# Performance work log

Measured on AMD Instinct MI355X. Metric: run time of the kernel, lower is better.

## Reference

```python
import jax, jax.numpy as jnp
import numpy as np

N_ATOMS = 100000
N_EDGES = 6400000
R_MAX = 6.0


def setup_inputs() -> dict:
    key = jax.random.key(0)
    k1, k2, k3 = jax.random.split(key, 3)
    R = jax.random.normal(k1, (N_ATOMS, 3), dtype=jnp.float32) * 10.0
    Z = jax.random.randint(k2, (N_ATOMS,), 1, 50, dtype=jnp.int32)
    idx = jax.random.randint(k3, (2, N_EDGES), 0, N_ATOMS, dtype=jnp.int32)
    # learned params (values per nn.initializers.constant in setup())
    a_exp = jnp.full((1,), 0.23, dtype=jnp.float32)
    a_num = jnp.full((1,), 0.4685, dtype=jnp.float32)
    coefficients = jnp.array([0.18175, 0.50986, 0.28022, 0.02817], dtype=jnp.float32)[:, None]
    exponents = jnp.array([3.1998, 0.94229, 0.4029, 0.20162], dtype=jnp.float32)[:, None]
    return {"R": R, "Z": Z, "idx": idx, "a_exp": a_exp, "a_num": a_num,
            "coefficients": coefficients, "exponents": exponents}


def reference(R, Z, idx, a_exp, a_num, coefficients, exponents):
    n_atoms = R.shape[0]
    idx_i, idx_j = idx[0], idx[1]
    Zf = Z.astype(R.dtype)
    Z_i, Z_j = Zf[idx_i], Zf[idx_j]                       # [E]
    dr_vec = R[idx_j] - R[idx_i]                          # free-space displacement [E,3]
    dr = jnp.sqrt(jnp.sum(dr_vec * dr_vec, axis=-1))      # [E]
    dr = jnp.clip(dr, 0.02, R_MAX)
    cos_cutoff = 0.5 * (jnp.cos(jnp.pi * dr / R_MAX) + 1.0)
    a_divisor = Z_i ** a_exp[0] + Z_j ** a_exp[0]
    dist = dr * a_divisor / a_num[0]                      # [E]
    f = jnp.sum(coefficients * jnp.exp(-exponents * dist), axis=0)  # (4,1)x[E]->(4,E)->[E]
    E_ij = 0.5 * Z_i * Z_j / dr * f * cos_cutoff          # [E]
    # mask_by_neighbor: padded edges carry idx == n_atoms -> zero contribution
    valid = (idx_i < n_atoms) & (idx_j < n_atoms)
    E_ij = jnp.where(valid, E_ij, 0.0)
    return jnp.sum(E_ij)
```

## Files before the change

### kernel.cpp

```cpp
#include <hip/hip_runtime.h>
#include <math.h>

#define N_ATOMS 100000
#define N_EDGES 6400000
#define NZB 50000
#define TBL_BYTES (N_ATOMS * 16)
#define XY_OFF    TBL_BYTES
#define Z_OFF     (XY_OFF + N_ATOMS)
#define WS_NEED   (Z_OFF + NZB)

__device__ __forceinline__ int cell6(float x) {
    return min(max((int)((x + 48.0f) * (1.0f / 6.0f)), 0), 15);
}

__global__ __launch_bounds__(256)
void build_tables(const float* __restrict__ R, const int* __restrict__ Z,
                  float4* __restrict__ P, unsigned char* __restrict__ gxy,
                  unsigned char* __restrict__ gz) {
    int i = blockIdx.x * blockDim.x + threadIdx.x;
    if (i < N_ATOMS) {
        float x = R[3 * i], y = R[3 * i + 1], z = R[3 * i + 2];
        P[i] = make_float4(x, y, z, (float)Z[i]);
        gxy[i] = (unsigned char)(cell6(x) | (cell6(y) << 4));
    }
    if (i < NZB) {
        int a0 = 2 * i, a1 = 2 * i + 1;
        int c0 = cell6(R[3 * a0 + 2]);
        int c1 = (a1 < N_ATOMS) ? cell6(R[3 * a1 + 2]) : 0;
        gz[i] = (unsigned char)(c0 | (c1 << 4));
    }
}

__global__ __launch_bounds__(1024)
void zbl_prefilter(const float4* __restrict__ P,
                   const unsigned char* __restrict__ gxy,
                   const unsigned char* __restrict__ gz,
                   const int*    __restrict__ idx,
                   const float*  __restrict__ a_exp,
                   const float*  __restrict__ a_num,
                   const float*  __restrict__ coef,
                   const float*  __restrict__ expo,
                   float*        __restrict__ out)
{
    __shared__ __align__(16) unsigned char sxy[N_ATOMS];
    __shared__ __align__(16) unsigned char sz[NZB];
    __shared__ float powz[64];
    __shared__ float wave_part[16];

    const int t = threadIdx.x;

    {
        const uint4* s = (const uint4*)gxy;
        uint4*       d = (uint4*)sxy;
        for (int k = t; k < N_ATOMS / 16; k += 1024) d[k] = s[k];
        const uint4* s2 = (const uint4*)gz;
        uint4*       d2 = (uint4*)sz;
        for (int k = t; k < NZB / 16; k += 1024) d2[k] = s2[k];
    }

    const float aexp     = a_exp[0];
    const float inv_anum = 1.0f / a_num[0];
    const float c0 = coef[0], c1 = coef[1], c2 = coef[2], c3 = coef[3];
    const float e0 = expo[0], e1 = expo[1], e2 = expo[2], e3 = expo[3];
    if (t < 64) powz[t] = __powf((float)t, aexp);
    __syncthreads();

    const int4* idx_i4 = (const int4*)idx;
    const int4* idx_j4 = (const int4*)(idx + N_EDGES);
    const int n4 = N_EDGES / 4;
    const int tid    = blockIdx.x * blockDim.x + t;
    const int stride = gridDim.x * blockDim.x;

    const float PI_OVER_RMAX = 0.52359877559829887f;

    float acc = 0.0f;
    for (int k = tid; k < n4; k += stride) {
        int4 ii = idx_i4[k];
        int4 jj = idx_j4[k];

        unsigned ia[4], jb[4];
        bool pass[4];
#pragma unroll
        for (int u = 0; u < 4; ++u) {
            int i = (&ii.x)[u];
            int j = (&jj.x)[u];
            bool valid = ((unsigned)i < N_ATOMS) & ((unsigned)j < N_ATOMS);
            unsigned a = min((unsigned)i, N_ATOMS - 1u);
            unsigned b = min((unsigned)j, N_ATOMS - 1u);
            ia[u] = a; jb[u] = b;
            int ci = sxy[a], cj = sxy[b];
            int dxy = abs((ci & 15) - (cj & 15)) | abs((ci >> 4) - (cj >> 4));
            pass[u] = valid & (dxy <= 1);
        }
#pragma unroll
        for (int u = 0; u < 4; ++u) {
            if (pass[u]) {
                unsigned a = ia[u], b = jb[u];
                int zi = (sz[a >> 1] >> ((a & 1) << 2)) & 15;
                int zj = (sz[b >> 1] >> ((b & 1) << 2)) & 15;
                if (abs(zi - zj) <= 1) {
                    float4 pa = P[a];
                    float4 pb = P[b];
                    float dx = pb.x - pa.x, dy = pb.y - pa.y, dz = pb.z - pa.z;
                    float d2 = dx * dx + dy * dy + dz * dz;
                    if (d2 < 36.0f) {
                        float dr = fmaxf(sqrtf(d2), 0.02f);
                        int za = (int)pa.w, zb = (int)pb.w;
                        float dist = dr * (powz[za & 63] + powz[zb & 63]) * inv_anum;
                        float f = c0 * __expf(-e0 * dist) + c1 * __expf(-e1 * dist)
                                + c2 * __expf(-e2 * dist) + c3 * __expf(-e3 * dist);
                        float cc = 0.5f * (__cosf(PI_OVER_RMAX * dr) + 1.0f);
                        acc += 0.5f * pa.w * pb.w / dr * f * cc;
                    }
                }
            }
        }
    }

#pragma unroll
    for (int off = 32; off > 0; off >>= 1)
        acc += __shfl_down(acc, off, 64);
    const int lane = t & 63;
    const int wave = t >> 6;
    if (lane == 0) wave_part[wave] = acc;
    __syncthreads();
    if (t == 0) {
        float s = 0.0f;
#pragma unroll
        for (int w = 0; w < 16; ++w) s += wave_part[w];
        atomicAdd(out, s);
    }
}

__global__ __launch_bounds__(256)
void zbl_mlp(const float4* __restrict__ P, const int* __restrict__ idx,
             const float* __restrict__ a_exp, const float* __restrict__ a_num,
             const float* __restrict__ coef, const float* __restrict__ expo,
             float* __restrict__ out)
{
    __shared__ float powz[64];
    __shared__ float wave_part[4];
    const float aexp = a_exp[0];
    const float inv_anum = 1.0f / a_num[0];
    const float c0 = coef[0], c1 = coef[1], c2 = coef[2], c3 = coef[3];
    const float e0 = expo[0], e1 = expo[1], e2 = expo[2], e3 = expo[3];
    const int t = threadIdx.x;
    if (t < 64) powz[t] = __powf((float)t, aexp);
    __syncthreads();
    const int4* idx_i4 = (const int4*)idx;
    const int4* idx_j4 = (const int4*)(idx + N_EDGES);
    const int n4 = N_EDGES / 4;
    const int tid = blockIdx.x * blockDim.x + t;
    const int stride = gridDim.x * blockDim.x;
    const float PI_OVER_RMAX = 0.52359877559829887f;
    float acc = 0.0f;
    for (int k = tid; k < n4; k += stride) {
        int4 ii = idx_i4[k];
        int4 jj = idx_j4[k];
        float4 pa[4], pb[4];
        bool valid[4];
#pragma unroll
        for (int u = 0; u < 4; ++u) {
            int i = (&ii.x)[u], j = (&jj.x)[u];
            valid[u] = ((unsigned)i < N_ATOMS) & ((unsigned)j < N_ATOMS);
            pa[u] = P[min((unsigned)i, N_ATOMS - 1u)];
            pb[u] = P[min((unsigned)j, N_ATOMS - 1u)];
        }
#pragma unroll
        for (int u = 0; u < 4; ++u) {
            float dx = pb[u].x - pa[u].x, dy = pb[u].y - pa[u].y, dz = pb[u].z - pa[u].z;
            float d2 = dx * dx + dy * dy + dz * dz;
            if (valid[u] && d2 < 36.0f) {
                float dr = fmaxf(sqrtf(d2), 0.02f);
                int zi = (int)pa[u].w, zj = (int)pb[u].w;
                float dist = dr * (powz[zi & 63] + powz[zj & 63]) * inv_anum;
                float f = c0 * __expf(-e0 * dist) + c1 * __expf(-e1 * dist)
                        + c2 * __expf(-e2 * dist) + c3 * __expf(-e3 * dist);
                float cc = 0.5f * (__cosf(PI_OVER_RMAX * dr) + 1.0f);
                acc += 0.5f * pa[u].w * pb[u].w / dr * f * cc;
            }
        }
    }
#pragma unroll
    for (int off = 32; off > 0; off >>= 1)
        acc += __shfl_down(acc, off, 64);
    const int lane = t & 63, wave = t >> 6;
    if (lane == 0) wave_part[wave] = acc;
    __syncthreads();
    if (t == 0)
        atomicAdd(out, wave_part[0] + wave_part[1] + wave_part[2] + wave_part[3]);
}

extern "C" void kernel_launch(void* const* d_in, const int* in_sizes, int n_in,
                              void* d_out, int out_size, void* d_ws, size_t ws_size,
                              hipStream_t stream) {
    const float* R     = (const float*)d_in[0];
    const int*   Z     = (const int*)d_in[1];
    const int*   idx   = (const int*)d_in[2];
    const float* a_exp = (const float*)d_in[3];
    const float* a_num = (const float*)d_in[4];
    const float* coef  = (const float*)d_in[5];
    const float* expo  = (const float*)d_in[6];
    float* out = (float*)d_out;

    hipMemsetAsync(out, 0, sizeof(float), stream);

    if (ws_size >= (size_t)WS_NEED) {
        float4*        P   = (float4*)d_ws;
        unsigned char* gxy = (unsigned char*)d_ws + XY_OFF;
        unsigned char* gz  = (unsigned char*)d_ws + Z_OFF;
        build_tables<<<(N_ATOMS + 255) / 256, 256, 0, stream>>>(R, Z, P, gxy, gz);
        zbl_prefilter<<<256, 1024, 0, stream>>>(P, gxy, gz, idx,
                                                a_exp, a_num, coef, expo, out);
    } else if (ws_size >= (size_t)TBL_BYTES) {
        float4* P = (float4*)d_ws;
        build_tables<<<(N_ATOMS + 255) / 256, 256, 0, stream>>>(
            R, Z, P, (unsigned char*)d_ws, (unsigned char*)d_ws);
        zbl_mlp<<<2048, 256, 0, stream>>>(P, idx, a_exp, a_num, coef, expo, out);
    }
}
```

Baseline: 122.0 us.

## Compact surviving edges into per-wave LDS queue to remove divergence

Drops the z-cell prefilter table and replaces the divergent per-lane evaluation with a per-wave ring queue in shared memory. Edges that pass the xy-cell test are compacted using ballot and popcount, and once 64 entries are queued the whole wave evaluates them together. This is meant to avoid running the costly exp/cos path with most lanes idle. In exchange it adds ballot and LDS traffic for every edge group, uses more shared memory, and sends more candidates to the full distance test because the z filter is gone.

```diff
diff --git a/kernel.cpp b/kernel.cpp
--- a/kernel.cpp
+++ b/kernel.cpp
@@ -3,11 +3,9 @@
 
 #define N_ATOMS 100000
 #define N_EDGES 6400000
-#define NZB 50000
 #define TBL_BYTES (N_ATOMS * 16)
 #define XY_OFF    TBL_BYTES
-#define Z_OFF     (XY_OFF + N_ATOMS)
-#define WS_NEED   (Z_OFF + NZB)
+#define WS_NEED   (XY_OFF + N_ATOMS)
 
 __device__ __forceinline__ int cell6(float x) {
     return min(max((int)((x + 48.0f) * (1.0f / 6.0f)), 0), 15);
@@ -15,35 +13,27 @@
 
 __global__ __launch_bounds__(256)
 void build_tables(const float* __restrict__ R, const int* __restrict__ Z,
-                  float4* __restrict__ P, unsigned char* __restrict__ gxy,
-                  unsigned char* __restrict__ gz) {
+                  float4* __restrict__ P, unsigned char* __restrict__ gxy) {
     int i = blockIdx.x * blockDim.x + threadIdx.x;
     if (i < N_ATOMS) {
         float x = R[3 * i], y = R[3 * i + 1], z = R[3 * i + 2];
         P[i] = make_float4(x, y, z, (float)Z[i]);
         gxy[i] = (unsigned char)(cell6(x) | (cell6(y) << 4));
     }
-    if (i < NZB) {
-        int a0 = 2 * i, a1 = 2 * i + 1;
-        int c0 = cell6(R[3 * a0 + 2]);
-        int c1 = (a1 < N_ATOMS) ? cell6(R[3 * a1 + 2]) : 0;
-        gz[i] = (unsigned char)(c0 | (c1 << 4));
-    }
 }
 
 __global__ __launch_bounds__(1024)
-void zbl_prefilter(const float4* __restrict__ P,
-                   const unsigned char* __restrict__ gxy,
-                   const unsigned char* __restrict__ gz,
-                   const int*    __restrict__ idx,
-                   const float*  __restrict__ a_exp,
-                   const float*  __restrict__ a_num,
-                   const float*  __restrict__ coef,
-                   const float*  __restrict__ expo,
-                   float*        __restrict__ out)
+void zbl_queue(const float4* __restrict__ P,
+               const unsigned char* __restrict__ gxy,
+               const int*    __restrict__ idx,
+               const float*  __restrict__ a_exp,
+               const float*  __restrict__ a_num,
+               const float*  __restrict__ coef,
+               const float*  __restrict__ expo,
+               float*        __restrict__ out)
 {
     __shared__ __align__(16) unsigned char sxy[N_ATOMS];
-    __shared__ __align__(16) unsigned char sz[NZB];
+    __shared__ uint2 q[16 * 128];
     __shared__ float powz[64];
     __shared__ float wave_part[16];
 
@@ -53,9 +43,6 @@
         const uint4* s = (const uint4*)gxy;
         uint4*       d = (uint4*)sxy;
         for (int k = t; k < N_ATOMS / 16; k += 1024) d[k] = s[k];
-        const uint4* s2 = (const uint4*)gz;
-        uint4*       d2 = (uint4*)sz;
-        for (int k = t; k < NZB / 16; k += 1024) d2[k] = s2[k];
     }
 
     const float aexp     = a_exp[0];
@@ -65,63 +52,91 @@
     if (t < 64) powz[t] = __powf((float)t, aexp);
     __syncthreads();
 
+    const int lane = t & 63;
+    const int wave = t >> 6;
+    uint2* myq = &q[wave << 7];
+
     const int4* idx_i4 = (const int4*)idx;
     const int4* idx_j4 = (const int4*)(idx + N_EDGES);
     const int n4 = N_EDGES / 4;
     const int tid    = blockIdx.x * blockDim.x + t;
     const int stride = gridDim.x * blockDim.x;
+    const int ITERS  = (n4 + stride - 1) / stride;
 
     const float PI_OVER_RMAX = 0.52359877559829887f;
-
+    const unsigned long long lmask = (1ull << lane) - 1ull;
+
+    unsigned qhead = 0, qtail = 0;
     float acc = 0.0f;
-    for (int k = tid; k < n4; k += stride) {
-        int4 ii = idx_i4[k];
-        int4 jj = idx_j4[k];
-
-        unsigned ia[4], jb[4];
-        bool pass[4];
+
+    for (int m = 0; m < ITERS; ++m) {
+        int k = tid + m * stride;
+        bool kv = k < n4;
+        int kc = kv ? k : (n4 - 1);
+        int4 ii = idx_i4[kc];
+        int4 jj = idx_j4[kc];
+
 #pragma unroll
         for (int u = 0; u < 4; ++u) {
             int i = (&ii.x)[u];
             int j = (&jj.x)[u];
-            bool valid = ((unsigned)i < N_ATOMS) & ((unsigned)j < N_ATOMS);
+            bool valid = kv & ((unsigned)i < N_ATOMS) & ((unsigned)j < N_ATOMS);
             unsigned a = min((unsigned)i, N_ATOMS - 1u);
             unsigned b = min((unsigned)j, N_ATOMS - 1u);
-            ia[u] = a; jb[u] = b;
             int ci = sxy[a], cj = sxy[b];
             int dxy = abs((ci & 15) - (cj & 15)) | abs((ci >> 4) - (cj >> 4));
-            pass[u] = valid & (dxy <= 1);
-        }
-#pragma unroll
-        for (int u = 0; u < 4; ++u) {
-            if (pass[u]) {
-                unsigned a = ia[u], b = jb[u];
-                int zi = (sz[a >> 1] >> ((a & 1) << 2)) & 15;
-                int zj = (sz[b >> 1] >> ((b & 1) << 2)) & 15;
-                if (abs(zi - zj) <= 1) {
-                    float4 pa = P[a];
-                    float4 pb = P[b];
-                    float dx = pb.x - pa.x, dy = pb.y - pa.y, dz = pb.z - pa.z;
-                    float d2 = dx * dx + dy * dy + dz * dz;
-                    if (d2 < 36.0f) {
-                        float dr = fmaxf(sqrtf(d2), 0.02f);
-                        int za = (int)pa.w, zb = (int)pb.w;
-                        float dist = dr * (powz[za & 63] + powz[zb & 63]) * inv_anum;
-                        float f = c0 * __expf(-e0 * dist) + c1 * __expf(-e1 * dist)
-                                + c2 * __expf(-e2 * dist) + c3 * __expf(-e3 * dist);
-                        float cc = 0.5f * (__cosf(PI_OVER_RMAX * dr) + 1.0f);
-                        acc += 0.5f * pa.w * pb.w / dr * f * cc;
-                    }
+            bool pass = valid & (dxy <= 1);
+
+            unsigned long long mk = __ballot(pass);
+            unsigned cnt   = (unsigned)__popcll(mk);
+            unsigned myoff = (unsigned)__popcll(mk & lmask);
+            if (pass) myq[(qtail + myoff) & 127] = make_uint2(a, b);
+            qtail += cnt;
+
+            if (qtail - qhead >= 64) {
+                uint2 e = myq[(qhead + lane) & 127];
+                qhead += 64;
+                float4 pi = P[e.x];
+                float4 pj = P[e.y];
+                float dx = pj.x - pi.x, dy = pj.y - pi.y, dz = pj.z - pi.z;
+                float d2 = dx * dx + dy * dy + dz * dz;
+                if (d2 < 36.0f) {
+                    float dr = fmaxf(sqrtf(d2), 0.02f);
+                    int zi = (int)pi.w, zj = (int)pj.w;
+                    float dist = dr * (powz[zi & 63] + powz[zj & 63]) * inv_anum;
+                    float f = c0 * __expf(-e0 * dist) + c1 * __expf(-e1 * dist)
+                            + c2 * __expf(-e2 * dist) + c3 * __expf(-e3 * dist);
+                    float cc = 0.5f * (__cosf(PI_OVER_RMAX * dr) + 1.0f);
+                    acc += 0.5f * pi.w * pj.w / dr * f * cc;
                 }
             }
         }
     }
 
+    while (qtail != qhead) {
+        unsigned n = min(64u, qtail - qhead);
+        if (lane < n) {
+            uint2 e = myq[(qhead + lane) & 127];
+            float4 pi = P[e.x];
+            float4 pj = P[e.y];
+            float dx = pj.x - pi.x, dy = pj.y - pi.y, dz = pj.z - pi.z;
+            float d2 = dx * dx + dy * dy + dz * dz;
+            if (d2 < 36.0f) {
+                float dr = fmaxf(sqrtf(d2), 0.02f);
+                int zi = (int)pi.w, zj = (int)pj.w;
+                float dist = dr * (powz[zi & 63] + powz[zj & 63]) * inv_anum;
+                float f = c0 * __expf(-e0 * dist) + c1 * __expf(-e1 * dist)
+                        + c2 * __expf(-e2 * dist) + c3 * __expf(-e3 * dist);
+                float cc = 0.5f * (__cosf(PI_OVER_RMAX * dr) + 1.0f);
+                acc += 0.5f * pi.w * pj.w / dr * f * cc;
+            }
+        }
+        qhead += n;
+    }
+
 #pragma unroll
     for (int off = 32; off > 0; off >>= 1)
         acc += __shfl_down(acc, off, 64);
-    const int lane = t & 63;
-    const int wave = t >> 6;
     if (lane == 0) wave_part[wave] = acc;
     __syncthreads();
     if (t == 0) {
@@ -208,14 +223,13 @@
     if (ws_size >= (size_t)WS_NEED) {
         float4*        P   = (float4*)d_ws;
         unsigned char* gxy = (unsigned char*)d_ws + XY_OFF;
-        unsigned char* gz  = (unsigned char*)d_ws + Z_OFF;
-        build_tables<<<(N_ATOMS + 255) / 256, 256, 0, stream>>>(R, Z, P, gxy, gz);
-        zbl_prefilter<<<256, 1024, 0, stream>>>(P, gxy, gz, idx,
-                                                a_exp, a_num, coef, expo, out);
+        build_tables<<<(N_ATOMS + 255) / 256, 256, 0, stream>>>(R, Z, P, gxy);
+        zbl_queue<<<256, 1024, 0, stream>>>(P, gxy, idx,
+                                            a_exp, a_num, coef, expo, out);
     } else if (ws_size >= (size_t)TBL_BYTES) {
         float4* P = (float4*)d_ws;
         build_tables<<<(N_ATOMS + 255) / 256, 256, 0, stream>>>(
-            R, Z, P, (unsigned char*)d_ws, (unsigned char*)d_ws);
+            R, Z, P, (unsigned char*)d_ws);
         zbl_mlp<<<2048, 256, 0, stream>>>(P, idx, a_exp, a_num, coef, expo, out);
     }
 }
```

After: 113.4 us. 7.1% less time.

## Compact surviving edges into per-wave LDS queue to remove divergence

Applied to the files above, without the earlier changes.

Edges that pass the grid-cell prefilter are now compacted with ballot/popcount into a 64-entry per-wave queue in shared memory. The full distance and energy evaluation runs only when the queue would overflow, so all lanes do useful work together. This targets the branch divergence where only a few lanes in a wave did the expensive body. In exchange it adds ballot, popcount and LDS traffic on every edge, plus extra shared memory on a block that already uses about 150KB of LDS.

```diff
diff --git a/kernel.cpp b/kernel.cpp
--- a/kernel.cpp
+++ b/kernel.cpp
@@ -31,19 +31,40 @@
     }
 }
 
+__device__ __forceinline__ float zbl_body(const float4* __restrict__ P,
+                                          const float* powz, uint2 e,
+                                          float inv_anum,
+                                          float c0, float c1, float c2, float c3,
+                                          float e0, float e1, float e2, float e3) {
+    const float PI_OVER_RMAX = 0.52359877559829887f;
+    float4 pi = P[e.x];
+    float4 pj = P[e.y];
+    float dx = pj.x - pi.x, dy = pj.y - pi.y, dz = pj.z - pi.z;
+    float d2 = dx * dx + dy * dy + dz * dz;
+    if (d2 >= 36.0f) return 0.0f;
+    float dr = fmaxf(sqrtf(d2), 0.02f);
+    int zi = (int)pi.w, zj = (int)pj.w;
+    float dist = dr * (powz[zi & 63] + powz[zj & 63]) * inv_anum;
+    float f = c0 * __expf(-e0 * dist) + c1 * __expf(-e1 * dist)
+            + c2 * __expf(-e2 * dist) + c3 * __expf(-e3 * dist);
+    float cc = 0.5f * (__cosf(PI_OVER_RMAX * dr) + 1.0f);
+    return 0.5f * pi.w * pj.w / dr * f * cc;
+}
+
 __global__ __launch_bounds__(1024)
-void zbl_prefilter(const float4* __restrict__ P,
-                   const unsigned char* __restrict__ gxy,
-                   const unsigned char* __restrict__ gz,
-                   const int*    __restrict__ idx,
-                   const float*  __restrict__ a_exp,
-                   const float*  __restrict__ a_num,
-                   const float*  __restrict__ coef,
-                   const float*  __restrict__ expo,
-                   float*        __restrict__ out)
+void zbl_qz(const float4* __restrict__ P,
+            const unsigned char* __restrict__ gxy,
+            const unsigned char* __restrict__ gz,
+            const int*    __restrict__ idx,
+            const float*  __restrict__ a_exp,
+            const float*  __restrict__ a_num,
+            const float*  __restrict__ coef,
+            const float*  __restrict__ expo,
+            float*        __restrict__ out)
 {
     __shared__ __align__(16) unsigned char sxy[N_ATOMS];
     __shared__ __align__(16) unsigned char sz[NZB];
+    __shared__ uint2 q[16 * 64];
     __shared__ float powz[64];
     __shared__ float wave_part[16];
 
@@ -65,63 +86,75 @@
     if (t < 64) powz[t] = __powf((float)t, aexp);
     __syncthreads();
 
+    const int lane = t & 63;
+    const int wave = t >> 6;
+    uint2* myq = &q[wave << 6];
+
     const int4* idx_i4 = (const int4*)idx;
     const int4* idx_j4 = (const int4*)(idx + N_EDGES);
     const int n4 = N_EDGES / 4;
     const int tid    = blockIdx.x * blockDim.x + t;
     const int stride = gridDim.x * blockDim.x;
-
-    const float PI_OVER_RMAX = 0.52359877559829887f;
-
+    const int ITERS  = (n4 + stride - 1) / stride;
+
+    const unsigned long long lmask = (1ull << lane) - 1ull;
+
+    unsigned qhead = 0, qtail = 0;
     float acc = 0.0f;
-    for (int k = tid; k < n4; k += stride) {
-        int4 ii = idx_i4[k];
-        int4 jj = idx_j4[k];
-
-        unsigned ia[4], jb[4];
-        bool pass[4];
+
+    for (int m = 0; m < ITERS; ++m) {
+        int k = tid + m * stride;
+        bool kv = k < n4;
+        int kc = kv ? k : (n4 - 1);
+        int4 ii = idx_i4[kc];
+        int4 jj = idx_j4[kc];
+
 #pragma unroll
         for (int u = 0; u < 4; ++u) {
             int i = (&ii.x)[u];
             int j = (&jj.x)[u];
-            bool valid = ((unsigned)i < N_ATOMS) & ((unsigned)j < N_ATOMS);
+            bool valid = kv & ((unsigned)i < N_ATOMS) & ((unsigned)j < N_ATOMS);
             unsigned a = min((unsigned)i, N_ATOMS - 1u);
             unsigned b = min((unsigned)j, N_ATOMS - 1u);
-            ia[u] = a; jb[u] = b;
             int ci = sxy[a], cj = sxy[b];
             int dxy = abs((ci & 15) - (cj & 15)) | abs((ci >> 4) - (cj >> 4));
-            pass[u] = valid & (dxy <= 1);
-        }
-#pragma unroll
-        for (int u = 0; u < 4; ++u) {
-            if (pass[u]) {
-                unsigned a = ia[u], b = jb[u];
-                int zi = (sz[a >> 1] >> ((a & 1) << 2)) & 15;
-                int zj = (sz[b >> 1] >> ((b & 1) << 2)) & 15;
-                if (abs(zi - zj) <= 1) {
-                    float4 pa = P[a];
-                    float4 pb = P[b];
-                    float dx = pb.x - pa.x, dy = pb.y - pa.y, dz = pb.z - pa.z;
-                    float d2 = dx * dx + dy * dy + dz * dz;
-                    if (d2 < 36.0f) {
-                        float dr = fmaxf(sqrtf(d2), 0.02f);
-                        int za = (int)pa.w, zb = (int)pb.w;
-                        float dist = dr * (powz[za & 63] + powz[zb & 63]) * inv_anum;
-                        float f = c0 * __expf(-e0 * dist) + c1 * __expf(-e1 * dist)
-                                + c2 * __expf(-e2 * dist) + c3 * __expf(-e3 * dist);
-                        float cc = 0.5f * (__cosf(PI_OVER_RMAX * dr) + 1.0f);
-                        acc += 0.5f * pa.w * pb.w / dr * f * cc;
-                    }
+            bool pxy = valid & (dxy <= 1);
+            unsigned aa = pxy ? (a >> 1) : 0u;
+            unsigned ba = pxy ? (b >> 1) : 0u;
+            int za = (sz[aa] >> ((a & 1) << 2)) & 15;
+            int zb = (sz[ba] >> ((b & 1) << 2)) & 15;
+            bool pass = pxy & (abs(za - zb) <= 1);
+
+            unsigned long long mk = __ballot(pass);
+            unsigned cnt   = (unsigned)__popcll(mk);
+            unsigned myoff = (unsigned)__popcll(mk & lmask);
+
+            unsigned pending = qtail - qhead;
+            if (pending + cnt > 64u) {
+                if (lane < (int)pending) {
+                    uint2 e = myq[(qhead + lane) & 63];
+                    acc += zbl_body(P, powz, e, inv_anum,
+                                    c0, c1, c2, c3, e0, e1, e2, e3);
                 }
+                qhead = qtail;
             }
+            if (pass) myq[(qtail + myoff) & 63] = make_uint2(a, b);
+            qtail += cnt;
+        }
+    }
+
+    {
+        unsigned pending = qtail - qhead;
+        if (lane < (int)pending) {
+            uint2 e = myq[(qhead + lane) & 63];
+            acc += zbl_body(P, powz, e, inv_anum,
+                            c0, c1, c2, c3, e0, e1, e2, e3);
         }
     }
 
 #pragma unroll
     for (int off = 32; off > 0; off >>= 1)
         acc += __shfl_down(acc, off, 64);
-    const int lane = t & 63;
-    const int wave = t >> 6;
     if (lane == 0) wave_part[wave] = acc;
     __syncthreads();
     if (t == 0) {
@@ -210,8 +243,8 @@
         unsigned char* gxy = (unsigned char*)d_ws + XY_OFF;
         unsigned char* gz  = (unsigned char*)d_ws + Z_OFF;
         build_tables<<<(N_ATOMS + 255) / 256, 256, 0, stream>>>(R, Z, P, gxy, gz);
-        zbl_prefilter<<<256, 1024, 0, stream>>>(P, gxy, gz, idx,
-                                                a_exp, a_num, coef, expo, out);
+        zbl_qz<<<256, 1024, 0, stream>>>(P, gxy, gz, idx,
+                                         a_exp, a_num, coef, expo, out);
     } else if (ws_size >= (size_t)TBL_BYTES) {
         float4* P = (float4*)d_ws;
         build_tables<<<(N_ATOMS + 255) / 256, 256, 0, stream>>>(
```

New measurement: 112.4 us. -7.9%, faster.
